# Optimization experiments

Measured on AMD Instinct MI355X. Metric: run time of the kernel, lower is better.

The kernel has to match this reference:

```python
import jax, jax.numpy as jnp
import numpy as np

D_MODEL = 768
EXPAND = 2
D_STATE = 128
HEADDIM = 64
D_CONV = 4
D_INNER = EXPAND * D_MODEL            # 1536
NHEADS = D_INNER // HEADDIM           # 24
CONV_DIM = D_INNER + 2 * D_STATE      # 1792
D_IN_PROJ = 2 * D_INNER + 2 * D_STATE + NHEADS  # 3352
EPS = 1e-5
BATCH, SEQLEN = 2, 2048


def silu(v):
    return v * jax.nn.sigmoid(v)


def mamba2(x, in_w, conv_w, conv_b, dt_bias, A_log, Dp, norm_w, out_w):
    # x: (b, l, d_model)
    b, l, _ = x.shape
    zxbcdt = x @ in_w.T                              # (b, l, d_in_proj)
    z = zxbcdt[..., :D_INNER]
    xBC = zxbcdt[..., D_INNER:D_INNER + CONV_DIM]
    dt = jax.nn.softplus(zxbcdt[..., D_INNER + CONV_DIM:] + dt_bias)  # (b, l, h)
    # causal depthwise conv1d, kernel D_CONV, left padding D_CONV-1
    pad = jnp.pad(xBC, ((0, 0), (D_CONV - 1, 0), (0, 0)))
    conv = conv_b
    for k in range(D_CONV):
        conv = conv + pad[:, k:k + l, :] * conv_w[:, k]
    xBC = silu(conv)
    xh = xBC[..., :D_INNER].reshape(b, l, NHEADS, HEADDIM)   # (b,l,h,p)
    Bm = xBC[..., D_INNER:D_INNER + D_STATE]                 # (b,l,n) ngroups=1
    Cm = xBC[..., D_INNER + D_STATE:]                        # (b,l,n)
    A = -jnp.exp(A_log)                                      # (h,)
    dA = jnp.exp(dt * A)                                     # (b,l,h)

    def step(h, inp):
        dA_t, dt_t, x_t, B_t, C_t = inp
        # h: (b, h, p, n)
        h = h * dA_t[:, :, None, None] + (dt_t[:, :, None] * x_t)[..., None] * B_t[:, None, None, :]
        y = jnp.einsum('bhpn,bn->bhp', h, C_t)
        return h, y

    h0 = jnp.zeros((b, NHEADS, HEADDIM, D_STATE), x.dtype)
    xs = (dA.transpose(1, 0, 2), dt.transpose(1, 0, 2), xh.transpose(1, 0, 2, 3),
          Bm.transpose(1, 0, 2), Cm.transpose(1, 0, 2))
    _, ys = jax.lax.scan(step, h0, xs)                       # (l,b,h,p)
    y = ys.transpose(1, 0, 2, 3) + Dp[None, None, :, None] * xh
    y = y.reshape(b, l, D_INNER)
    # RMSNormGated (norm_before_gate=False): rmsnorm(y * silu(z)) * weight
    y = y * silu(z)
    y = y * jax.lax.rsqrt(jnp.mean(jnp.square(y), axis=-1, keepdims=True) + EPS) * norm_w
    return y @ out_w.T


def setup_inputs() -> dict:
    key = jax.random.key(0)
    ks = jax.random.split(key, 9)
    s = 0.02
    return {
        'x': jax.random.normal(ks[0], (BATCH, SEQLEN, D_MODEL), jnp.float32),
        'in_proj_w': jax.random.normal(ks[1], (2, D_IN_PROJ, D_MODEL), jnp.float32) * s,
        'conv_w': jax.random.normal(ks[2], (2, CONV_DIM, D_CONV), jnp.float32) * 0.2,
        'conv_b': jax.random.normal(ks[3], (2, CONV_DIM), jnp.float32) * s,
        'dt_bias': jax.random.normal(ks[4], (2, NHEADS), jnp.float32) * 0.1,
        'A_log': jnp.log(jax.random.uniform(ks[5], (2, NHEADS), jnp.float32, 1.0, 16.0)),
        'D': jax.random.normal(ks[6], (2, NHEADS), jnp.float32) * 0.5 + 1.0,
        'norm_w': jnp.ones((2, D_INNER), jnp.float32),
        'out_proj_w': jax.random.normal(ks[7], (2, D_MODEL, D_INNER), jnp.float32) * s,
    }


def reference(x, in_proj_w, conv_w, conv_b, dt_bias, A_log, D, norm_w, out_proj_w):
    h_fwd = mamba2(x, in_proj_w[0], conv_w[0], conv_b[0], dt_bias[0], A_log[0], D[0], norm_w[0], out_proj_w[0])
    x_rev = jnp.flip(x, axis=1)
    h_bwd_rev = mamba2(x_rev, in_proj_w[1], conv_w[1], conv_b[1], dt_bias[1], A_log[1], D[1], norm_w[1], out_proj_w[1])
    return h_fwd + jnp.flip(h_bwd_rev, axis=1)
```

## Files before the change

### kernel.cpp

```cpp
#include <hip/hip_runtime.h>
#include <hip/hip_bf16.h>

typedef __attribute__((ext_vector_type(8))) short short8;
typedef __attribute__((ext_vector_type(4))) short bfx4;
typedef __attribute__((ext_vector_type(4))) float floatx4;

#define SEQ     2048
#define DMODEL  768
#define DINNER  1536
#define DSTATE  128
#define NH      24
#define CONVDIM 1792
#define NPROJ   3352
#define QCH     64
#define NCH     (SEQ / QCH)

__device__ inline float bf2f(short s) {
    return __uint_as_float(((unsigned)(unsigned short)s) << 16);
}
__device__ inline short f2bf(float f) {
    __hip_bfloat16 h = __float2bfloat16(f);
    return *reinterpret_cast<short*>(&h);
}
__device__ inline void gl_lds16(const void* g, void* l) {
    __builtin_amdgcn_global_load_lds((const __attribute__((address_space(1))) unsigned int*)g,
                                     (__attribute__((address_space(3))) unsigned int*)l, 16, 0, 0);
}

__global__ __launch_bounds__(256) void cvt_kernel(const float* __restrict__ src,
                                                  __hip_bfloat16* __restrict__ dst, int n4) {
    int i = blockIdx.x * 256 + threadIdx.x;
    if (i >= n4) return;
    float4 v = *(const float4*)(src + (size_t)i * 4);
    bfx4 o = { f2bf(v.x), f2bf(v.y), f2bf(v.z), f2bf(v.w) };
    *(bfx4*)((short*)dst + (size_t)i * 4) = o;
}

__global__ __launch_bounds__(256) void gemm_bt(const __hip_bfloat16* __restrict__ Abase, size_t aStride,
                                               const __hip_bfloat16* __restrict__ Bbase, size_t bStride,
                                               float* __restrict__ C,
                                               __hip_bfloat16* __restrict__ Zb,
                                               __hip_bfloat16* __restrict__ Xb,
                                               float* __restrict__ DT,
                                               float* __restrict__ LA,
                                               const float* __restrict__ dtbias,
                                               const float* __restrict__ Alog,
                                               int M, int N, int K, int zdiv, int mode, int flipA) {
    __shared__ short As[3][64 * 64];
    __shared__ short Bs[3][64 * 64];
    int tid = threadIdx.x;
    int w = tid >> 6, lane = tid & 63;
    int q = lane >> 4, mm = lane & 15;
    int wm = w >> 1, wn = w & 1;
    int m0 = blockIdx.x * 128, n0 = blockIdx.y * 128;
    int z = blockIdx.z;
    int dir = z / zdiv, ks = z - dir * zdiv;
    int kl = K / zdiv;
    int kbeg = ks * kl;
    const short* Ag = (const short*)Abase + (size_t)dir * aStride;
    const short* Bg = (const short*)Bbase + (size_t)dir * bStride;
    int fA = flipA && dir;

    size_t aoff[2], boff[2];
    int ldso[2];
#pragma unroll
    for (int j = 0; j < 2; j++) {
        int widx = w * 2 + j;
        int ln = widx * 8 + (lane >> 3);
        int s  = lane & 7;
        int c  = s ^ (ln & 7);
        int row = (c < 4) ? ln : ln + 64;
        int ch  = (c < 4) ? c : (c ^ 4);
        int ar = m0 + row;
        if (fA) { int bb = ar >> 11, tt = ar & 2047; ar = (bb << 11) + (2047 - tt); }
        aoff[j] = (size_t)ar * K + ch * 8;
        int br = n0 + row; if (br > N - 1) br = N - 1;
        boff[j] = (size_t)br * K + ch * 8;
        ldso[j] = widx * 1024;
    }

    floatx4 acc[16];
#pragma unroll
    for (int i = 0; i < 16; i++) acc[i] = (floatx4){0.f, 0.f, 0.f, 0.f};

    int niter = kl / 32;
    auto stage = [&](int buf, int k0) {
#pragma unroll
        for (int j = 0; j < 2; j++) {
            gl_lds16(Ag + aoff[j] + kbeg + k0, (char*)&As[buf][0] + ldso[j]);
            gl_lds16(Bg + boff[j] + kbeg + k0, (char*)&Bs[buf][0] + ldso[j]);
        }
    };
    stage(0, 0);
    if (niter > 1) stage(1, 32);
    int slotA = (q ^ (mm & 7) ^ (wm << 2)) * 8;
    int slotB = (q ^ (mm & 7) ^ (wn << 2)) * 8;
    for (int it = 0; it < niter; it++) {
        if (it + 1 < niter) asm volatile("s_waitcnt vmcnt(4)" ::: "memory");
        else                asm volatile("s_waitcnt vmcnt(0)" ::: "memory");
        __builtin_amdgcn_s_barrier();
        __builtin_amdgcn_sched_barrier(0);
        if (it + 2 < niter) stage((it + 2) % 3, (it + 2) * 32);
        int bsel = it % 3;
        const short* Ab = &As[bsel][0];
        const short* Bb = &Bs[bsel][0];
        short8 af[4], bfr[4];
#pragma unroll
        for (int mb = 0; mb < 4; mb++)
            af[mb] = *(const short8*)&Ab[(mb * 16 + mm) * 64 + slotA];
#pragma unroll
        for (int nb = 0; nb < 4; nb++)
            bfr[nb] = *(const short8*)&Bb[(nb * 16 + mm) * 64 + slotB];
        __builtin_amdgcn_s_setprio(1);
#pragma unroll
        for (int mb = 0; mb < 4; mb++)
#pragma unroll
            for (int nb = 0; nb < 4; nb++)
                acc[mb * 4 + nb] = __builtin_amdgcn_mfma_f32_16x16x32_bf16(af[mb], bfr[nb], acc[mb * 4 + nb], 0, 0, 0);
        __builtin_amdgcn_s_setprio(0);
    }

    __hip_bfloat16* Zb2 = Zb + (size_t)dir * 4096 * DINNER;
    __hip_bfloat16* Xb2 = Xb + (size_t)dir * 4096 * CONVDIM;
    float* DT2 = DT + (size_t)dir * 4096 * NH;
    float* LA2 = LA + (size_t)dir * 4096 * NH;
    const float* dtb2 = dtbias + dir * NH;
    const float* Al2  = Alog + dir * NH;

#pragma unroll
    for (int mb = 0; mb < 4; mb++) {
#pragma unroll
        for (int nb = 0; nb < 4; nb++) {
            int col = n0 + wn * 64 + nb * 16 + mm;
            if (col >= N) continue;
#pragma unroll
            for (int r = 0; r < 4; r++) {
                int rr = m0 + wm * 64 + mb * 16 + q * 4 + r;
                float v = acc[mb * 4 + nb][r];
                if (mode == 1) {
                    int orow = rr;
                    if (dir) { int b = rr >> 11, t = rr & 2047; orow = (b << 11) + (2047 - t); }
                    atomicAdd(&C[(size_t)orow * N + col], v);
                } else {
                    if (col < DINNER) {
                        Zb2[(size_t)rr * DINNER + col] = __float2bfloat16(v);
                    } else if (col < DINNER + CONVDIM) {
                        Xb2[(size_t)rr * CONVDIM + (col - DINNER)] = __float2bfloat16(v);
                    } else {
                        int hh = col - (DINNER + CONVDIM);
                        float raw = v + dtb2[hh];
                        float dtv = (raw > 20.f) ? raw : log1pf(__expf(raw));
                        float Av  = -__expf(Al2[hh]);
                        DT2[(size_t)rr * NH + hh] = dtv;
                        LA2[(size_t)rr * NH + hh] = dtv * Av;
                    }
                }
            }
        }
    }
}

__global__ __launch_bounds__(256) void conv_kernel(const __hip_bfloat16* __restrict__ Xb,
                                                   const float* __restrict__ conv_w,
                                                   const float* __restrict__ conv_b,
                                                   __hip_bfloat16* __restrict__ xh,
                                                   __hip_bfloat16* __restrict__ Bm,
                                                   __hip_bfloat16* __restrict__ Cm) {
    int db  = blockIdx.x >> 7;
    int dir = db >> 1;
    int t0  = (blockIdx.x & 127) * 16;
    int c8  = threadIdx.x * 8;
    if (c8 >= CONVDIM) return;

    float wk[4][8], bs[8];
#pragma unroll
    for (int j = 0; j < 8; j++) {
        bs[j] = conv_b[dir * CONVDIM + c8 + j];
#pragma unroll
        for (int k = 0; k < 4; k++) wk[k][j] = conv_w[((size_t)dir * CONVDIM + c8 + j) * 4 + k];
    }

    const short* xrow = (const short*)Xb + (size_t)db * SEQ * CONVDIM + c8;
    short8 win[4];
    const short8 zer = {0, 0, 0, 0, 0, 0, 0, 0};
#pragma unroll
    for (int k = 0; k < 3; k++) {
        int ts = t0 - 3 + k;
        win[k] = (ts >= 0) ? *(const short8*)(xrow + (size_t)ts * CONVDIM) : zer;
    }

    for (int tt = 0; tt < 16; tt++) {
        int t = t0 + tt;
        win[3] = *(const short8*)(xrow + (size_t)t * CONVDIM);
        short8 outv;
#pragma unroll
        for (int j = 0; j < 8; j++) {
            float acc = bs[j];
#pragma unroll
            for (int k = 0; k < 4; k++) acc += wk[k][j] * bf2f(win[k][j]);
            float sv = acc / (1.f + __expf(-acc));
            outv[j] = f2bf(sv);
        }
        if (c8 < DINNER)
            *(short8*)((short*)xh + (size_t)(db * SEQ + t) * DINNER + c8) = outv;
        else if (c8 < DINNER + DSTATE)
            *(short8*)((short*)Bm + (size_t)(db * SEQ + t) * DSTATE + (c8 - DINNER)) = outv;
        else
            *(short8*)((short*)Cm + (size_t)(db * SEQ + t) * DSTATE + (c8 - DINNER - DSTATE)) = outv;
        win[0] = win[1]; win[1] = win[2]; win[2] = win[3];
    }
}

__global__ __launch_bounds__(256) void ssd1_kernel(const __hip_bfloat16* __restrict__ XH,
                                                   const __hip_bfloat16* __restrict__ BMh,
                                                   const float* __restrict__ DT,
                                                   const float* __restrict__ LA,
                                                   short* __restrict__ SS,
                                                   float* __restrict__ CUM) {
    int blk = blockIdx.x;
    int ck = blk & 31;
    int dbh = blk >> 5;
    int hh = dbh % NH, db = dbh / NH;
    int base_row = db * SEQ + ck * QCH;

    __shared__ float cum_s[QCH], dt_s[QCH];
    __shared__ short Xt[64][72];
    __shared__ short Bt[128][72];

    int tid = threadIdx.x;
    int lane = tid & 63, w = tid >> 6;
    int q = lane >> 4, mm = lane & 15;

    if (tid < QCH) {
        float la  = LA[(size_t)(base_row + tid) * NH + hh];
        float dtv = DT[(size_t)(base_row + tid) * NH + hh];
        float cs = la;
#pragma unroll
        for (int d = 1; d < 64; d <<= 1) {
            float u = __shfl_up(cs, d);
            if (tid >= d) cs += u;
        }
        cum_s[tid] = cs;
        dt_s[tid] = dtv;
        CUM[(size_t)dbh * SEQ + ck * QCH + tid] = cs;
    }
    __syncthreads();
    float cumL = cum_s[QCH - 1];

    {
        int s2 = (tid & 31) * 2, pb = tid >> 5;
        float f0 = dt_s[s2]     * __expf(cumL - cum_s[s2]);
        float f1 = dt_s[s2 + 1] * __expf(cumL - cum_s[s2 + 1]);
        const short* r0 = (const short*)XH + (size_t)(base_row + s2) * DINNER + hh * 64 + pb * 8;
        const short* r1 = r0 + DINNER;
        short8 x0 = *(const short8*)r0;
        short8 x1 = *(const short8*)r1;
#pragma unroll
        for (int j = 0; j < 8; j++) {
            unsigned lo = (unsigned short)f2bf(f0 * bf2f(x0[j]));
            unsigned hi = (unsigned short)f2bf(f1 * bf2f(x1[j]));
            *(unsigned*)&Xt[pb * 8 + j][s2] = lo | (hi << 16);
        }
    }
    {
        int s2 = (tid & 31) * 2, nb = tid >> 5;
        const short* r0 = (const short*)BMh + (size_t)(base_row + s2) * DSTATE + nb * 16;
        const short* r1 = r0 + DSTATE;
        short8 b0a = *(const short8*)r0,  b0b = *(const short8*)(r0 + 8);
        short8 b1a = *(const short8*)r1,  b1b = *(const short8*)(r1 + 8);
#pragma unroll
        for (int j = 0; j < 8; j++) {
            *(unsigned*)&Bt[nb * 16 + j][s2] =
                (unsigned)(unsigned short)b0a[j] | ((unsigned)(unsigned short)b1a[j] << 16);
            *(unsigned*)&Bt[nb * 16 + 8 + j][s2] =
                (unsigned)(unsigned short)b0b[j] | ((unsigned)(unsigned short)b1b[j] << 16);
        }
    }
    __syncthreads();

    floatx4 acc[8];
#pragma unroll
    for (int i = 0; i < 8; i++) acc[i] = (floatx4){0.f, 0.f, 0.f, 0.f};
#pragma unroll
    for (int kk = 0; kk < 2; kk++) {
        short8 a = *(const short8*)&Xt[w * 16 + mm][kk * 32 + q * 8];
#pragma unroll
        for (int cb = 0; cb < 8; cb++) {
            short8 b = *(const short8*)&Bt[cb * 16 + mm][kk * 32 + q * 8];
            acc[cb] = __builtin_amdgcn_mfma_f32_16x16x32_bf16(a, b, acc[cb], 0, 0, 0);
        }
    }
    short* Sp = SS + (size_t)blk * 8192;
#pragma unroll
    for (int cb = 0; cb < 8; cb++)
#pragma unroll
        for (int r = 0; r < 4; r++)
            Sp[(w * 16 + q * 4 + r) * DSTATE + cb * 16 + mm] = f2bf(acc[cb][r]);
}

__global__ __launch_bounds__(256) void ssd2_kernel(const short* __restrict__ SS,
                                                   const float* __restrict__ CUM,
                                                   short* __restrict__ Hprev) {
    int blk = blockIdx.x;
    int dbh = blk >> 2, part = blk & 3;
    int off = part * 2048 + threadIdx.x * 8;
    size_t base = (size_t)dbh * NCH * 8192 + off;
    float h[8];
#pragma unroll
    for (int j = 0; j < 8; j++) h[j] = 0.f;
    for (int c = 0; c < NCH; c++) {
        float W = __expf(CUM[(size_t)dbh * SEQ + c * QCH + QCH - 1]);
        size_t p = base + (size_t)c * 8192;
        short8 s = *(const short8*)(SS + p);
        short8 o;
#pragma unroll
        for (int j = 0; j < 8; j++) o[j] = f2bf(h[j]);
        *(short8*)(Hprev + p) = o;
#pragma unroll
        for (int j = 0; j < 8; j++) h[j] = fmaf(h[j], W, bf2f(s[j]));
    }
}

__global__ __launch_bounds__(256) void ssd3_kernel(const __hip_bfloat16* __restrict__ XH,
                                                   const __hip_bfloat16* __restrict__ BMh,
                                                   const __hip_bfloat16* __restrict__ CMh,
                                                   const float* __restrict__ DT,
                                                   const float* __restrict__ CUM,
                                                   const short* __restrict__ Hprev,
                                                   __hip_bfloat16* __restrict__ Yb) {
    int blk = blockIdx.x;
    int ck = blk & 31;
    int dbh = blk >> 5;
    int hh = dbh % NH, db = dbh / NH;
    int base_row = db * SEQ + ck * QCH;

    __shared__ float cum_s[QCH], dt_s[QCH];
    __shared__ short Ct[64][136];
    __shared__ short G[64][72];
    __shared__ short Xt[64][72];

    int tid = threadIdx.x;
    int lane = tid & 63, w = tid >> 6;
    int q = lane >> 4, mm = lane & 15;

    if (tid < QCH) {
        cum_s[tid] = CUM[(size_t)dbh * SEQ + ck * QCH + tid];
        dt_s[tid]  = DT[(size_t)(base_row + tid) * NH + hh];
    }

    const short* Cg = (const short*)CMh + (size_t)base_row * DSTATE;
    const short* Bg = (const short*)BMh + (size_t)base_row * DSTATE;
    floatx4 P[4];
#pragma unroll
    for (int i = 0; i < 4; i++) P[i] = (floatx4){0.f, 0.f, 0.f, 0.f};
#pragma unroll
    for (int kk = 0; kk < 4; kk++) {
        short8 a = *(const short8*)(Cg + (size_t)(w * 16 + mm) * DSTATE + kk * 32 + q * 8);
#pragma unroll
        for (int cb = 0; cb < 4; cb++) {
            short8 b = *(const short8*)(Bg + (size_t)(cb * 16 + mm) * DSTATE + kk * 32 + q * 8);
            P[cb] = __builtin_amdgcn_mfma_f32_16x16x32_bf16(a, b, P[cb], 0, 0, 0);
        }
    }
    __syncthreads();

    {
        int t = tid & 63, nb4 = tid >> 6;
        float wt = __expf(cum_s[t]);
        const short* src = Cg + (size_t)t * DSTATE + nb4 * 32;
#pragma unroll
        for (int u = 0; u < 2; u++) {
            short8 v = *(const short8*)(src + u * 16);
            short8 v2 = *(const short8*)(src + u * 16 + 8);
#pragma unroll
            for (int j = 0; j < 4; j++) {
                unsigned lo = (unsigned short)f2bf(wt * bf2f(v[2 * j]));
                unsigned hi = (unsigned short)f2bf(wt * bf2f(v[2 * j + 1]));
                *(unsigned*)&Ct[t][nb4 * 32 + u * 16 + 2 * j] = lo | (hi << 16);
                lo = (unsigned short)f2bf(wt * bf2f(v2[2 * j]));
                hi = (unsigned short)f2bf(wt * bf2f(v2[2 * j + 1]));
                *(unsigned*)&Ct[t][nb4 * 32 + u * 16 + 8 + 2 * j] = lo | (hi << 16);
            }
        }
    }
    {
        int s2 = (tid & 31) * 2, pb = tid >> 5;
        const short* r0 = (const short*)XH + (size_t)(base_row + s2) * DINNER + hh * 64 + pb * 8;
        const short* r1 = r0 + DINNER;
        short8 x0 = *(const short8*)r0;
        short8 x1 = *(const short8*)r1;
#pragma unroll
        for (int j = 0; j < 8; j++) {
            *(unsigned*)&Xt[pb * 8 + j][s2] =
                (unsigned)(unsigned short)x0[j] | ((unsigned)(unsigned short)x1[j] << 16);
        }
    }
#pragma unroll
    for (int cb = 0; cb < 4; cb++) {
#pragma unroll
        for (int r = 0; r < 4; r++) {
            int t = w * 16 + q * 4 + r;
            int s = cb * 16 + mm;
            float g = (s <= t) ? P[cb][r] * __expf(cum_s[t] - cum_s[s]) * dt_s[s] : 0.f;
            G[t][s] = f2bf(g);
        }
    }
    __syncthreads();

    floatx4 Y[4];
#pragma unroll
    for (int i = 0; i < 4; i++) Y[i] = (floatx4){0.f, 0.f, 0.f, 0.f};
#pragma unroll
    for (int kk = 0; kk < 2; kk++) {
        short8 a = *(const short8*)&G[w * 16 + mm][kk * 32 + q * 8];
#pragma unroll
        for (int cb = 0; cb < 4; cb++) {
            short8 b = *(const short8*)&Xt[cb * 16 + mm][kk * 32 + q * 8];
            Y[cb] = __builtin_amdgcn_mfma_f32_16x16x32_bf16(a, b, Y[cb], 0, 0, 0);
        }
    }
    const short* Hc = Hprev + (size_t)blk * 8192;
#pragma unroll
    for (int kk = 0; kk < 4; kk++) {
        short8 a = *(const short8*)&Ct[w * 16 + mm][kk * 32 + q * 8];
#pragma unroll
        for (int cb = 0; cb < 4; cb++) {
            short8 b = *(const short8*)(Hc + (size_t)(cb * 16 + mm) * DSTATE + kk * 32 + q * 8);
            Y[cb] = __builtin_amdgcn_mfma_f32_16x16x32_bf16(a, b, Y[cb], 0, 0, 0);
        }
    }
#pragma unroll
    for (int cb = 0; cb < 4; cb++)
#pragma unroll
        for (int r = 0; r < 4; r++)
            Yb[(size_t)(base_row + w * 16 + q * 4 + r) * DINNER + hh * 64 + cb * 16 + mm] =
                __float2bfloat16(Y[cb][r]);
}

__global__ __launch_bounds__(192) void gate_kernel(const __hip_bfloat16* __restrict__ Yb,
                                                   const __hip_bfloat16* __restrict__ xh,
                                                   const __hip_bfloat16* __restrict__ Zb,
                                                   const float* __restrict__ Dp,
                                                   const float* __restrict__ norm_w,
                                                   __hip_bfloat16* __restrict__ A2) {
    int row = blockIdx.x;
    int dir = row >> 12;
    int c8 = threadIdx.x * 8;
    int hd = c8 >> 6;
    const short* yr = (const short*)Yb + (size_t)row * DINNER + c8;
    const short* xr = (const short*)xh + (size_t)row * DINNER + c8;
    const short* zr = (const short*)Zb + (size_t)row * DINNER + c8;

    short8 y8 = *(const short8*)yr;
    short8 x8 = *(const short8*)xr;
    short8 z8 = *(const short8*)zr;
    float Dv = Dp[dir * NH + hd];

    float vals[8];
    float ss = 0.f;
#pragma unroll
    for (int j = 0; j < 8; j++) {
        float v = bf2f(y8[j]) + Dv * bf2f(x8[j]);
        float z = bf2f(z8[j]);
        v *= z / (1.f + __expf(-z));
        vals[j] = v;
        ss += v * v;
    }
#pragma unroll
    for (int off = 32; off; off >>= 1) ss += __shfl_down(ss, off);
    __shared__ float ls[3];
    if ((threadIdx.x & 63) == 0) ls[threadIdx.x >> 6] = ss;
    __syncthreads();
    float tot = ls[0] + ls[1] + ls[2];
    float scale = rsqrtf(tot / (float)DINNER + 1e-5f);

    const float* nw = norm_w + dir * DINNER + c8;
    short8 o;
#pragma unroll
    for (int j = 0; j < 8; j++) o[j] = f2bf(vals[j] * scale * nw[j]);
    *(short8*)((short*)A2 + (size_t)row * DINNER + c8) = o;
}

extern "C" void kernel_launch(void* const* d_in, const int* in_sizes, int n_in,
                              void* d_out, int out_size, void* d_ws, size_t ws_size,
                              hipStream_t stream) {
    const float* x        = (const float*)d_in[0];
    const float* in_w     = (const float*)d_in[1];
    const float* conv_w   = (const float*)d_in[2];
    const float* conv_b   = (const float*)d_in[3];
    const float* dt_bias  = (const float*)d_in[4];
    const float* A_log    = (const float*)d_in[5];
    const float* Dp       = (const float*)d_in[6];
    const float* norm_w   = (const float*)d_in[7];
    const float* out_w    = (const float*)d_in[8];
    float* out = (float*)d_out;

    const size_t szW2 = (size_t)2 * DMODEL * DINNER * 2;
    const size_t szZ  = (size_t)8192 * DINNER * 2;
    const size_t szXH = (size_t)8192 * DINNER * 2;
    const size_t szBM = (size_t)8192 * DSTATE * 2;
    const size_t szCM = szBM;
    const size_t szDT = (size_t)8192 * NH * 4;
    const size_t szLA = szDT;
    const size_t szA1 = (size_t)4096 * DMODEL * 2;
    const size_t szW1 = (size_t)2 * NPROJ * DMODEL * 2;
    const size_t szXB = (size_t)8192 * CONVDIM * 2;
    const size_t szYb = (size_t)8192 * DINNER * 2;
    const size_t szSS = (size_t)96 * NCH * 8192 * 2;
    const size_t szRa = szA1 + szW1 + szXB;
    size_t szR = szRa;
    if (szR < szYb) szR = szYb;
    if (szR < szSS) szR = szSS;
    const size_t szHp = szSS;
    const size_t szCU = (size_t)96 * SEQ * 4;

    char* ws = (char*)d_ws;
    size_t off = 0;
    auto alloc = [&](size_t bytes) { char* p = ws + off; off += (bytes + 255) & ~(size_t)255; return p; };

    __hip_bfloat16* W2 = (__hip_bfloat16*)alloc(szW2);
    __hip_bfloat16* Z  = (__hip_bfloat16*)alloc(szZ);
    __hip_bfloat16* XH = (__hip_bfloat16*)alloc(szXH);
    __hip_bfloat16* BM = (__hip_bfloat16*)alloc(szBM);
    __hip_bfloat16* CM = (__hip_bfloat16*)alloc(szCM);
    float* DT = (float*)alloc(szDT);
    float* LA = (float*)alloc(szLA);
    char*  R  = (char*)alloc(szR);
    __hip_bfloat16* A1  = (__hip_bfloat16*)R;
    __hip_bfloat16* W1  = (__hip_bfloat16*)(R + szA1);
    __hip_bfloat16* XBC = (__hip_bfloat16*)(R + szA1 + szW1);
    short* SS = (short*)R;
    __hip_bfloat16* Yb = (__hip_bfloat16*)R;

    short* Hp = (short*)alloc(szHp);
    float* CU = (float*)alloc(szCU);
    if (off > ws_size) return;

    int n1 = 2 * NPROJ * DMODEL / 4;
    cvt_kernel<<<(n1 + 255) / 256, 256, 0, stream>>>(in_w, W1, n1);
    int n2 = 2 * DMODEL * DINNER / 4;
    cvt_kernel<<<(n2 + 255) / 256, 256, 0, stream>>>(out_w, W2, n2);
    int n3 = 4096 * DMODEL / 4;
    cvt_kernel<<<(n3 + 255) / 256, 256, 0, stream>>>(x, A1, n3);

    {
        dim3 grid(4096 / 128, (NPROJ + 127) / 128, 2);
        gemm_bt<<<grid, 256, 0, stream>>>(A1, 0,
                                          W1, (size_t)NPROJ * DMODEL,
                                          nullptr, Z, XBC, DT, LA, dt_bias, A_log,
                                          4096, NPROJ, DMODEL, 1, 2, 1);
    }

    conv_kernel<<<4 * 128, 256, 0, stream>>>(XBC, conv_w, conv_b, XH, BM, CM);

    ssd1_kernel<<<4 * NH * NCH, 256, 0, stream>>>(XH, BM, DT, LA, SS, CU);
    ssd2_kernel<<<4 * NH * 4, 256, 0, stream>>>(SS, CU, Hp);
    ssd3_kernel<<<4 * NH * NCH, 256, 0, stream>>>(XH, BM, CM, DT, CU, Hp, Yb);

    gate_kernel<<<2 * 4096, 192, 0, stream>>>(Yb, XH, Z, Dp, norm_w, Z);

    hipMemsetAsync(out, 0, (size_t)4096 * DMODEL * 4, stream);
    {
        dim3 grid(4096 / 128, DMODEL / 128, 4);
        gemm_bt<<<grid, 256, 0, stream>>>(Z, (size_t)4096 * DINNER,
                                          W2, (size_t)DMODEL * DINNER,
                                          out, nullptr, nullptr, nullptr, nullptr, nullptr, nullptr,
                                          4096, DMODEL, DINNER, 2, 1, 0);
    }
}
```

Before: 390.3 us.

## Add 256x256-tile 8-wave in-projection GEMM with 4-stage pipelined LDS loads

```diff
diff --git a/kernel.cpp b/kernel.cpp
--- a/kernel.cpp
+++ b/kernel.cpp
@@ -36,16 +36,141 @@
     *(bfx4*)((short*)dst + (size_t)i * 4) = o;
 }
 
+__global__ __launch_bounds__(512, 2) void gemm_in_256(const __hip_bfloat16* __restrict__ Abase,
+                                                      const __hip_bfloat16* __restrict__ Bbase, size_t bStride,
+                                                      __hip_bfloat16* __restrict__ Zb,
+                                                      __hip_bfloat16* __restrict__ Xb,
+                                                      float* __restrict__ DT,
+                                                      float* __restrict__ LA,
+                                                      const float* __restrict__ dtbias,
+                                                      const float* __restrict__ Alog,
+                                                      int N, int K) {
+    __shared__ short As[4][8192];
+    __shared__ short Bs[4][8192];
+    int tid = threadIdx.x;
+    int w = tid >> 6, lane = tid & 63;
+    int q = lane >> 4, mm = lane & 15;
+    int wm = w >> 2, wn = w & 3;
+    int m0 = blockIdx.x * 256, n0 = blockIdx.y * 256;
+    int dir = blockIdx.z;
+    const short* Ag = (const short*)Abase;
+    const short* Bg = (const short*)Bbase + (size_t)dir * bStride;
+
+    int ln  = w * 8 + (lane >> 3);
+    int sl  = lane & 7;
+    int cc  = sl ^ (ln & 7);
+    int lrow = (cc < 4) ? ln : ln + 64;
+    int chk  = (cc < 4) ? cc : (cc ^ 4);
+    size_t aoff[2], boff[2];
+#pragma unroll
+    for (int h = 0; h < 2; h++) {
+        int ar = m0 + h * 128 + lrow;
+        if (dir) { int bb = ar >> 11, tt = ar & 2047; ar = (bb << 11) + (2047 - tt); }
+        aoff[h] = (size_t)ar * K + chk * 8;
+        int br = n0 + h * 128 + lrow; if (br > N - 1) br = N - 1;
+        boff[h] = (size_t)br * K + chk * 8;
+    }
+
+    floatx4 acc[32];
+#pragma unroll
+    for (int i = 0; i < 32; i++) acc[i] = (floatx4){0.f, 0.f, 0.f, 0.f};
+
+    int nkt = K / 32;
+    auto stageA = [&](int buf, int kt, int h) {
+        gl_lds16(Ag + aoff[h] + kt * 32, (char*)&As[buf][h * 4096 + w * 512]);
+    };
+    auto stageB = [&](int buf, int kt, int h) {
+        gl_lds16(Bg + boff[h] + kt * 32, (char*)&Bs[buf][h * 4096 + w * 512]);
+    };
+#pragma unroll
+    for (int kt = 0; kt < 3; kt++) {
+        stageA(kt, kt, 0); stageA(kt, kt, 1);
+        stageB(kt, kt, 0); stageB(kt, kt, 1);
+    }
+    asm volatile("s_waitcnt vmcnt(8)" ::: "memory");
+    __builtin_amdgcn_s_barrier();
+
+    int slotB = (q ^ (mm & 7) ^ ((wn & 1) << 2)) * 8;
+    int slotA0 = (q ^ (mm & 7)) * 8;
+    int bunit = (wn >> 1) * 4096;
+
+    for (int kt = 0; kt < nkt; kt++) {
+        int buf = kt & 3;
+        const short* Ab = &As[buf][wm * 4096];
+        const short* Bb = &Bs[buf][bunit];
+        int issue = (kt + 3 < nkt);
+        if (issue) { stageA((kt + 3) & 3, kt + 3, 0); stageA((kt + 3) & 3, kt + 3, 1); }
+        short8 b8[4];
+#pragma unroll
+        for (int nb = 0; nb < 4; nb++)
+            b8[nb] = *(const short8*)&Bb[(nb * 16 + mm) * 64 + slotB];
+        short8 a8[4];
+#pragma unroll
+        for (int i = 0; i < 4; i++)
+            a8[i] = *(const short8*)&Ab[(i * 16 + mm) * 64 + slotA0];
+        __builtin_amdgcn_s_setprio(1);
+#pragma unroll
+        for (int i = 0; i < 4; i++)
+#pragma unroll
+            for (int nb = 0; nb < 4; nb++)
+                acc[i * 4 + nb] = __builtin_amdgcn_mfma_f32_16x16x32_bf16(a8[i], b8[nb], acc[i * 4 + nb], 0, 0, 0);
+        __builtin_amdgcn_s_setprio(0);
+        __builtin_amdgcn_s_barrier();
+        if (issue) { stageB((kt + 3) & 3, kt + 3, 0); stageB((kt + 3) & 3, kt + 3, 1); }
+#pragma unroll
+        for (int i = 0; i < 4; i++)
+            a8[i] = *(const short8*)&Ab[(i * 16 + mm) * 64 + (slotA0 ^ 32)];
+        __builtin_amdgcn_s_setprio(1);
+#pragma unroll
+        for (int i = 0; i < 4; i++)
+#pragma unroll
+            for (int nb = 0; nb < 4; nb++)
+                acc[16 + i * 4 + nb] = __builtin_amdgcn_mfma_f32_16x16x32_bf16(a8[i], b8[nb], acc[16 + i * 4 + nb], 0, 0, 0);
+        __builtin_amdgcn_s_setprio(0);
+        if (kt + 3 < nkt)      asm volatile("s_waitcnt vmcnt(8)" ::: "memory");
+        else if (kt + 2 < nkt) asm volatile("s_waitcnt vmcnt(4)" ::: "memory");
+        else if (kt + 1 < nkt) asm volatile("s_waitcnt vmcnt(0)" ::: "memory");
+        __builtin_amdgcn_s_barrier();
+    }
+
+    __hip_bfloat16* Zb2 = Zb + (size_t)dir * 4096 * DINNER;
+    __hip_bfloat16* Xb2 = Xb + (size_t)dir * 4096 * CONVDIM;
+    float* DT2 = DT + (size_t)dir * 4096 * NH;
+    float* LA2 = LA + (size_t)dir * 4096 * NH;
+    const float* dtb2 = dtbias + dir * NH;
+    const float* Al2  = Alog + dir * NH;
+
+#pragma unroll
+    for (int mb = 0; mb < 8; mb++) {
+#pragma unroll
+        for (int nb = 0; nb < 4; nb++) {
+            int col = n0 + wn * 64 + nb * 16 + mm;
+            if (col >= N) continue;
+#pragma unroll
+            for (int r = 0; r < 4; r++) {
+                int rr = m0 + wm * 128 + mb * 16 + q * 4 + r;
+                float v = acc[mb * 4 + nb][r];
+                if (col < DINNER) {
+                    Zb2[(size_t)rr * DINNER + col] = __float2bfloat16(v);
+                } else if (col < DINNER + CONVDIM) {
+                    Xb2[(size_t)rr * CONVDIM + (col - DINNER)] = __float2bfloat16(v);
+                } else {
+                    int hh = col - (DINNER + CONVDIM);
+                    float raw = v + dtb2[hh];
+                    float dtv = (raw > 20.f) ? raw : log1pf(__expf(raw));
+                    float Av  = -__expf(Al2[hh]);
+                    DT2[(size_t)rr * NH + hh] = dtv;
+                    LA2[(size_t)rr * NH + hh] = dtv * Av;
+                }
+            }
+        }
+    }
+}
+
 __global__ __launch_bounds__(256) void gemm_bt(const __hip_bfloat16* __restrict__ Abase, size_t aStride,
                                                const __hip_bfloat16* __restrict__ Bbase, size_t bStride,
                                                float* __restrict__ C,
-                                               __hip_bfloat16* __restrict__ Zb,
-                                               __hip_bfloat16* __restrict__ Xb,
-                                               float* __restrict__ DT,
-                                               float* __restrict__ LA,
-                                               const float* __restrict__ dtbias,
-                                               const float* __restrict__ Alog,
-                                               int M, int N, int K, int zdiv, int mode, int flipA) {
+                                               int M, int N, int K, int zdiv) {
     __shared__ short As[3][64 * 64];
     __shared__ short Bs[3][64 * 64];
     int tid = threadIdx.x;
@@ -59,7 +184,6 @@
     int kbeg = ks * kl;
     const short* Ag = (const short*)Abase + (size_t)dir * aStride;
     const short* Bg = (const short*)Bbase + (size_t)dir * bStride;
-    int fA = flipA && dir;
 
     size_t aoff[2], boff[2];
     int ldso[2];
@@ -72,7 +196,6 @@
         int row = (c < 4) ? ln : ln + 64;
         int ch  = (c < 4) ? c : (c ^ 4);
         int ar = m0 + row;
-        if (fA) { int bb = ar >> 11, tt = ar & 2047; ar = (bb << 11) + (2047 - tt); }
         aoff[j] = (size_t)ar * K + ch * 8;
         int br = n0 + row; if (br > N - 1) br = N - 1;
         boff[j] = (size_t)br * K + ch * 8;
@@ -120,13 +243,6 @@
         __builtin_amdgcn_s_setprio(0);
     }
 
-    __hip_bfloat16* Zb2 = Zb + (size_t)dir * 4096 * DINNER;
-    __hip_bfloat16* Xb2 = Xb + (size_t)dir * 4096 * CONVDIM;
-    float* DT2 = DT + (size_t)dir * 4096 * NH;
-    float* LA2 = LA + (size_t)dir * 4096 * NH;
-    const float* dtb2 = dtbias + dir * NH;
-    const float* Al2  = Alog + dir * NH;
-
 #pragma unroll
     for (int mb = 0; mb < 4; mb++) {
 #pragma unroll
@@ -137,24 +253,9 @@
             for (int r = 0; r < 4; r++) {
                 int rr = m0 + wm * 64 + mb * 16 + q * 4 + r;
                 float v = acc[mb * 4 + nb][r];
-                if (mode == 1) {
-                    int orow = rr;
-                    if (dir) { int b = rr >> 11, t = rr & 2047; orow = (b << 11) + (2047 - t); }
-                    atomicAdd(&C[(size_t)orow * N + col], v);
-                } else {
-                    if (col < DINNER) {
-                        Zb2[(size_t)rr * DINNER + col] = __float2bfloat16(v);
-                    } else if (col < DINNER + CONVDIM) {
-                        Xb2[(size_t)rr * CONVDIM + (col - DINNER)] = __float2bfloat16(v);
-                    } else {
-                        int hh = col - (DINNER + CONVDIM);
-                        float raw = v + dtb2[hh];
-                        float dtv = (raw > 20.f) ? raw : log1pf(__expf(raw));
-                        float Av  = -__expf(Al2[hh]);
-                        DT2[(size_t)rr * NH + hh] = dtv;
-                        LA2[(size_t)rr * NH + hh] = dtv * Av;
-                    }
-                }
+                int orow = rr;
+                if (dir) { int b = rr >> 11, t = rr & 2047; orow = (b << 11) + (2047 - t); }
+                atomicAdd(&C[(size_t)orow * N + col], v);
             }
         }
     }
@@ -544,11 +645,11 @@
     cvt_kernel<<<(n3 + 255) / 256, 256, 0, stream>>>(x, A1, n3);
 
     {
-        dim3 grid(4096 / 128, (NPROJ + 127) / 128, 2);
-        gemm_bt<<<grid, 256, 0, stream>>>(A1, 0,
-                                          W1, (size_t)NPROJ * DMODEL,
-                                          nullptr, Z, XBC, DT, LA, dt_bias, A_log,
-                                          4096, NPROJ, DMODEL, 1, 2, 1);
+        dim3 grid(4096 / 256, (NPROJ + 255) / 256, 2);
+        gemm_in_256<<<grid, 512, 0, stream>>>(A1,
+                                              W1, (size_t)NPROJ * DMODEL,
+                                              Z, XBC, DT, LA, dt_bias, A_log,
+                                              NPROJ, DMODEL);
     }
 
     conv_kernel<<<4 * 128, 256, 0, stream>>>(XBC, conv_w, conv_b, XH, BM, CM);
@@ -564,7 +665,7 @@
         dim3 grid(4096 / 128, DMODEL / 128, 4);
         gemm_bt<<<grid, 256, 0, stream>>>(Z, (size_t)4096 * DINNER,
                                           W2, (size_t)DMODEL * DINNER,
-                                          out, nullptr, nullptr, nullptr, nullptr, nullptr, nullptr,
-                                          4096, DMODEL, DINNER, 2, 1, 0);
-    }
-}
+                                          out,
+                                          4096, DMODEL, DINNER, 2);
+    }
+}
```

Result: slower. 418.5 us (+7.2%).
